# Performance work log

Measured on AMD Instinct MI355X. Metric: run time of the kernel, lower is better.

## Reference

```python
import jax, jax.numpy as jnp
import numpy as np

N_NODES = 100000
N_EDGES = 1000000
VOCAB = 105
OUT_DIM = 16
HIDDEN = 128


def setup_inputs() -> dict:
    key = jax.random.key(0)
    ks = jax.random.split(key, 9)
    x = jax.random.randint(ks[0], (N_NODES,), 0, VOCAB)
    pair_basis = jax.random.normal(ks[1], (N_EDGES, OUT_DIM), dtype=jnp.float32)
    i = jax.random.randint(ks[2], (N_EDGES,), 0, N_NODES)
    j = jax.random.randint(ks[3], (N_EDGES,), 0, N_NODES)
    # parameters
    emb_table = jax.random.normal(ks[4], (VOCAB, HIDDEN), dtype=jnp.float32)
    W_pair = jax.random.normal(ks[5], (OUT_DIM, HIDDEN), dtype=jnp.float32) / np.sqrt(OUT_DIM)
    b_pair = jnp.zeros((HIDDEN,), dtype=jnp.float32)
    W_emb = jax.random.normal(ks[6], (3 * HIDDEN, HIDDEN), dtype=jnp.float32) / np.sqrt(3 * HIDDEN)
    b_emb = jnp.zeros((HIDDEN,), dtype=jnp.float32)
    return {
        "x": x, "pair_basis": pair_basis, "i": i, "j": j,
        "emb_table": emb_table, "W_pair": W_pair, "b_pair": b_pair,
        "W_emb": W_emb, "b_emb": b_emb,
    }


def reference(x, pair_basis, i, j, emb_table, W_pair, b_pair, W_emb, b_emb):
    xe = emb_table[x]                                   # [N_nodes, H] embedding lookup
    pb = jax.nn.silu(pair_basis @ W_pair + b_pair)      # [E, H]
    inp = jnp.concatenate([xe[i], xe[j], pb], axis=-1)  # [E, 3H]
    emb = jax.nn.silu(inp @ W_emb + b_emb)              # [E, H]
    return emb
```

## Files before the change

### kernel.cpp

```cpp
#include <hip/hip_runtime.h>
#include <hip/hip_bf16.h>

#define N_EDGES 1000000
#define HID 128
#define VOC 105

#define WSU_T   0
#define WSU_U   (VOC * HID)
#define WSU_W3  (2 * VOC * HID)
#define WSU_WP  (WSU_W3 + 16384)
#define WSU_TU  (2 * VOC * HID)
#define WSB_VI  ((WSU_WP + 4096) * 2)
#define WSB_VJ  (WSB_VI + N_EDGES)

typedef float    f32x4 __attribute__((ext_vector_type(4)));
typedef _Float16 f16x8 __attribute__((ext_vector_type(8)));
typedef _Float16 f16x4 __attribute__((ext_vector_type(4)));

static __device__ __forceinline__ f16x8 as_f16x8(f32x4 v) {
    return __builtin_bit_cast(f16x8, v);
}
static __device__ __forceinline__ unsigned int pk2(float a, float b) {
    return __builtin_bit_cast(unsigned int, __builtin_amdgcn_cvt_pkrtz(a, b));
}

__global__ void prep_kernel(const int*   __restrict__ xv,
                            const int*   __restrict__ ii,
                            const int*   __restrict__ jj,
                            const float* __restrict__ emb_table,
                            const float* __restrict__ W_pair,
                            const float* __restrict__ b_pair,
                            const float* __restrict__ W_emb,
                            const float* __restrict__ b_emb,
                            char* __restrict__ wsb) {
    _Float16* ws = (_Float16*)wsb;
    int b = blockIdx.x, t = threadIdx.x;
    if (b < VOC) {
        int v = b, which = t >> 7, h = t & 127;
        const float* wr = W_emb + which * HID * HID;
        const float* ev = emb_table + v * HID;
        float acc = which ? 0.f : b_emb[h];
        for (int d = 0; d < HID; ++d) acc = fmaf(ev[d], wr[d * HID + h], acc);
        ws[(which ? WSU_U : WSU_T) + v * HID + h] = (_Float16)acc;
    } else if (b < VOC + 64) {
        int idx = (b - VOC) * 256 + t;
        int tt = idx & 7, lane = (idx >> 3) & 63, q = idx >> 9;
        int ks = q >> 3, nf = q & 7;
        int hl = 16 * (tt >> 2) + 4 * (lane >> 4) + (tt & 3);
        int k = 32 * ks + hl;
        int p = lane & 15;
        int n = (nf < 4) ? (4 * p + nf) : (64 + 4 * p + (nf - 4));
        ws[WSU_W3 + idx] = (_Float16)W_emb[(2 * HID + k) * HID + n];
    } else if (b < VOC + 64 + 16) {
        int idx = (b - VOC - 64) * 256 + t;
        int tt = idx & 7, lane = (idx >> 3) & 63, hf = idx >> 9;
        int k = 8 * (lane >> 4) + tt;
        int h = 16 * hf + (lane & 15);
        float v = (k < 16) ? W_pair[k * HID + h] : (k == 16 ? b_pair[h] : 0.f);
        ws[WSU_WP + idx] = (_Float16)v;
    } else {
        int e4 = ((b - VOC - 64 - 16) * 256 + t) * 4;
        if (e4 < N_EDGES) {
            int4 iv = *(const int4*)(ii + e4);
            int4 jv = *(const int4*)(jj + e4);
            unsigned int vi = (unsigned)xv[iv.x] | ((unsigned)xv[iv.y] << 8) |
                              ((unsigned)xv[iv.z] << 16) | ((unsigned)xv[iv.w] << 24);
            unsigned int vj = (unsigned)xv[jv.x] | ((unsigned)xv[jv.y] << 8) |
                              ((unsigned)xv[jv.z] << 16) | ((unsigned)xv[jv.w] << 24);
            *(unsigned int*)(wsb + WSB_VI + e4) = vi;
            *(unsigned int*)(wsb + WSB_VJ + e4) = vj;
        }
    }
}

__device__ __forceinline__ float silu_f(float x) {
    return x * __builtin_amdgcn_rcpf(1.f + __builtin_amdgcn_exp2f(-1.44269504088896341f * x));
}

__global__ __launch_bounds__(256, 2) void edge_kernel(
    const float* __restrict__ pair_basis,
    const char*  __restrict__ wsb,
    float* __restrict__ out)
{
    __shared__ __align__(16) _Float16 sTU[WSU_TU];
    const _Float16* ws = (const _Float16*)wsb;
    const int tid = threadIdx.x;
    {
        const uint4* src = (const uint4*)ws;
        uint4* dst = (uint4*)sTU;
        for (int c = tid; c < (WSU_TU * 2 / 16); c += 256) dst[c] = src[c];
    }
    const int lane = tid & 63;
    const int w    = tid >> 6;
    const int m    = lane & 15;
    const int g    = lane >> 4;

    f32x4 wpf[8];
    #pragma unroll
    for (int hf = 0; hf < 8; ++hf)
        wpf[hf] = *(const f32x4*)(ws + WSU_WP + (hf * 64 + lane) * 8);
    f32x4 w3r[32];
    #pragma unroll
    for (int q = 0; q < 32; ++q)
        w3r[q] = *(const f32x4*)(ws + WSU_W3 + (q * 64 + lane) * 8);
    #pragma unroll
    for (int hf = 0; hf < 8; ++hf) asm volatile("" : "+v"(wpf[hf]));
    #pragma unroll
    for (int q = 0; q < 32; ++q)  asm volatile("" : "+v"(w3r[q]));
    __syncthreads();

    const _Float16* sT  = sTU;
    const _Float16* sU  = sTU + WSU_U;
    const unsigned char* viB = (const unsigned char*)(wsb + WSB_VI);
    const unsigned char* vjB = (const unsigned char*)(wsb + WSB_VJ);

    const int ntiles = N_EDGES / 64;
    const int gstep  = (int)gridDim.x;

    int tile = blockIdx.x;
    if (tile >= ntiles) return;

    f32x4 p0 = {0,0,0,0}, p1 = {0,0,0,0};
    unsigned int viq, vjq;
    {
        int e0 = tile * 64 + w * 16;
        if (g < 2) {
            const f32x4* pr = (const f32x4*)(pair_basis + (size_t)(e0 + m) * 16 + g * 8);
            p0 = __builtin_nontemporal_load(pr);
            p1 = __builtin_nontemporal_load(pr + 1);
        }
        viq = *(const unsigned int*)(viB + e0 + 4 * g);
        vjq = *(const unsigned int*)(vjB + e0 + 4 * g);
    }

    while (true) {
        const int e0 = tile * 64 + w * 16;
        const int nt = tile + gstep;

        f32x4 q0 = {0,0,0,0}, q1 = {0,0,0,0};
        unsigned int nvi = 0, nvj = 0;
        if (nt < ntiles) {
            int ne0 = nt * 64 + w * 16;
            if (g < 2) {
                const f32x4* pr = (const f32x4*)(pair_basis + (size_t)(ne0 + m) * 16 + g * 8);
                q0 = __builtin_nontemporal_load(pr);
                q1 = __builtin_nontemporal_load(pr + 1);
            }
            nvi = *(const unsigned int*)(viB + ne0 + 4 * g);
            nvj = *(const unsigned int*)(vjB + ne0 + 4 * g);
        }

        f16x8 b2 = {0, 0, 0, 0, 0, 0, 0, 0};
        if (g < 2) {
            uint4 packed = {pk2(p0[0], p0[1]), pk2(p0[2], p0[3]),
                            pk2(p1[0], p1[1]), pk2(p1[2], p1[3])};
            b2 = __builtin_bit_cast(f16x8, packed);
        } else if (g == 2) {
            b2[0] = (_Float16)1.0f;
        }

        f16x8 a2[4];
        const f32x4 zero = {0.f, 0.f, 0.f, 0.f};
        #pragma unroll
        for (int ks = 0; ks < 4; ++ks) {
            f32x4 dA = __builtin_amdgcn_mfma_f32_16x16x32_f16(as_f16x8(wpf[2 * ks]),     b2, zero, 0, 0, 0);
            f32x4 dB = __builtin_amdgcn_mfma_f32_16x16x32_f16(as_f16x8(wpf[2 * ks + 1]), b2, zero, 0, 0, 0);
            uint4 packed;
            packed.x = pk2(silu_f(dA[0]), silu_f(dA[1]));
            packed.y = pk2(silu_f(dA[2]), silu_f(dA[3]));
            packed.z = pk2(silu_f(dB[0]), silu_f(dB[1]));
            packed.w = pk2(silu_f(dB[2]), silu_f(dB[3]));
            a2[ks] = __builtin_bit_cast(f16x8, packed);
        }

        f32x4 acc[8];
        #pragma unroll
        for (int r = 0; r < 4; ++r) {
            int vi = (viq >> (8 * r)) & 0xff;
            int vj = (vjq >> (8 * r)) & 0xff;
            f16x4 tlo = *(const f16x4*)(sT + vi * HID + 4 * m);
            f16x4 thi = *(const f16x4*)(sT + vi * HID + 64 + 4 * m);
            f16x4 ulo = *(const f16x4*)(sU + vj * HID + 4 * m);
            f16x4 uhi = *(const f16x4*)(sU + vj * HID + 64 + 4 * m);
            f16x4 slo = tlo + ulo;
            f16x4 shi = thi + uhi;
            #pragma unroll
            for (int nf = 0; nf < 4; ++nf) {
                acc[nf][r]     = (float)slo[nf];
                acc[4 + nf][r] = (float)shi[nf];
            }
        }

        #pragma unroll
        for (int ks = 0; ks < 4; ++ks) {
            #pragma unroll
            for (int nf = 0; nf < 8; ++nf)
                acc[nf] = __builtin_amdgcn_mfma_f32_16x16x32_f16(a2[ks], as_f16x8(w3r[ks * 8 + nf]), acc[nf], 0, 0, 0);
        }

        #pragma unroll
        for (int r = 0; r < 4; ++r) {
            float* op = out + (size_t)(e0 + 4 * g + r) * HID + 4 * m;
            f32x4 o0, o1;
            #pragma unroll
            for (int nf = 0; nf < 4; ++nf) {
                o0[nf] = silu_f(acc[nf][r]);
                o1[nf] = silu_f(acc[4 + nf][r]);
            }
            __builtin_nontemporal_store(o0, (f32x4*)op);
            __builtin_nontemporal_store(o1, (f32x4*)(op + 64));
        }

        if (nt >= ntiles) break;
        tile = nt; p0 = q0; p1 = q1; viq = nvi; vjq = nvj;
    }
}

extern "C" void kernel_launch(void* const* d_in, const int* in_sizes, int n_in,
                              void* d_out, int out_size, void* d_ws, size_t ws_size,
                              hipStream_t stream) {
    const int*   x          = (const int*)d_in[0];
    const float* pair_basis = (const float*)d_in[1];
    const int*   ii         = (const int*)d_in[2];
    const int*   jj         = (const int*)d_in[3];
    const float* emb_table  = (const float*)d_in[4];
    const float* W_pair     = (const float*)d_in[5];
    const float* b_pair     = (const float*)d_in[6];
    const float* W_emb      = (const float*)d_in[7];
    const float* b_emb      = (const float*)d_in[8];
    char* wsb = (char*)d_ws;
    float* out = (float*)d_out;

    const int ngather = (N_EDGES + 1023) / 1024;
    prep_kernel<<<VOC + 64 + 16 + ngather, 256, 0, stream>>>(
        x, ii, jj, emb_table, W_pair, b_pair, W_emb, b_emb, wsb);
    edge_kernel<<<512, 256, 0, stream>>>(pair_basis, wsb, out);
}
```

Baseline: 147.9 us.

## Move W_emb fragments from registers to LDS and use 1024-thread blocks

The 32 W3 weight fragments that were held in registers (128 VGPRs per thread) are now staged in shared memory together with the T/U tables and W_pair, and are read from LDS inside the MFMA loop. Blocks grow to 1024 threads (16 waves), with launch bounds of 4 blocks per unit, and the grid drops to 256 blocks, each wave striding over 16-edge tiles on its own. The aim is to cut register pressure so more waves fit and memory latency for the store-bound output is better hidden. In exchange, every tile now does extra LDS reads for the weights, and the larger LDS footprint per block may limit occupancy.

```diff
diff --git a/kernel.cpp b/kernel.cpp
--- a/kernel.cpp
+++ b/kernel.cpp
@@ -9,8 +9,8 @@
 #define WSU_U   (VOC * HID)
 #define WSU_W3  (2 * VOC * HID)
 #define WSU_WP  (WSU_W3 + 16384)
-#define WSU_TU  (2 * VOC * HID)
-#define WSB_VI  ((WSU_WP + 4096) * 2)
+#define WSU_ALL (WSU_WP + 4096)
+#define WSB_VI  (WSU_ALL * 2)
 #define WSB_VJ  (WSB_VI + N_EDGES)
 
 typedef float    f32x4 __attribute__((ext_vector_type(4)));
@@ -77,53 +77,48 @@
     return x * __builtin_amdgcn_rcpf(1.f + __builtin_amdgcn_exp2f(-1.44269504088896341f * x));
 }
 
-__global__ __launch_bounds__(256, 2) void edge_kernel(
+__global__ __launch_bounds__(1024, 4) void edge_kernel(
     const float* __restrict__ pair_basis,
     const char*  __restrict__ wsb,
     float* __restrict__ out)
 {
-    __shared__ __align__(16) _Float16 sTU[WSU_TU];
+    __shared__ __align__(16) _Float16 sAll[WSU_ALL];
     const _Float16* ws = (const _Float16*)wsb;
     const int tid = threadIdx.x;
     {
         const uint4* src = (const uint4*)ws;
-        uint4* dst = (uint4*)sTU;
-        for (int c = tid; c < (WSU_TU * 2 / 16); c += 256) dst[c] = src[c];
+        uint4* dst = (uint4*)sAll;
+        for (int c = tid; c < (WSU_ALL * 2 / 16); c += 1024) dst[c] = src[c];
     }
     const int lane = tid & 63;
     const int w    = tid >> 6;
     const int m    = lane & 15;
     const int g    = lane >> 4;
 
+    const _Float16* sT  = sAll;
+    const _Float16* sU  = sAll + WSU_U;
+    const _Float16* sW3 = sAll + WSU_W3;
+    const _Float16* sWP = sAll + WSU_WP;
+    const unsigned char* viB = (const unsigned char*)(wsb + WSB_VI);
+    const unsigned char* vjB = (const unsigned char*)(wsb + WSB_VJ);
+    __syncthreads();
+
     f32x4 wpf[8];
     #pragma unroll
     for (int hf = 0; hf < 8; ++hf)
-        wpf[hf] = *(const f32x4*)(ws + WSU_WP + (hf * 64 + lane) * 8);
-    f32x4 w3r[32];
-    #pragma unroll
-    for (int q = 0; q < 32; ++q)
-        w3r[q] = *(const f32x4*)(ws + WSU_W3 + (q * 64 + lane) * 8);
+        wpf[hf] = *(const f32x4*)(sWP + (hf * 64 + lane) * 8);
     #pragma unroll
     for (int hf = 0; hf < 8; ++hf) asm volatile("" : "+v"(wpf[hf]));
-    #pragma unroll
-    for (int q = 0; q < 32; ++q)  asm volatile("" : "+v"(w3r[q]));
-    __syncthreads();
-
-    const _Float16* sT  = sTU;
-    const _Float16* sU  = sTU + WSU_U;
-    const unsigned char* viB = (const unsigned char*)(wsb + WSB_VI);
-    const unsigned char* vjB = (const unsigned char*)(wsb + WSB_VJ);
-
-    const int ntiles = N_EDGES / 64;
-    const int gstep  = (int)gridDim.x;
-
-    int tile = blockIdx.x;
-    if (tile >= ntiles) return;
+
+    const int nwt   = N_EDGES / 16;
+    const int wstep = (int)gridDim.x * 16;
+    int wt = blockIdx.x * 16 + w;
+    if (wt >= nwt) return;
 
     f32x4 p0 = {0,0,0,0}, p1 = {0,0,0,0};
     unsigned int viq, vjq;
     {
-        int e0 = tile * 64 + w * 16;
+        int e0 = wt * 16;
         if (g < 2) {
             const f32x4* pr = (const f32x4*)(pair_basis + (size_t)(e0 + m) * 16 + g * 8);
             p0 = __builtin_nontemporal_load(pr);
@@ -134,13 +129,13 @@
     }
 
     while (true) {
-        const int e0 = tile * 64 + w * 16;
-        const int nt = tile + gstep;
+        const int e0 = wt * 16;
+        const int nt = wt + wstep;
 
         f32x4 q0 = {0,0,0,0}, q1 = {0,0,0,0};
         unsigned int nvi = 0, nvj = 0;
-        if (nt < ntiles) {
-            int ne0 = nt * 64 + w * 16;
+        if (nt < nwt) {
+            int ne0 = nt * 16;
             if (g < 2) {
                 const f32x4* pr = (const f32x4*)(pair_basis + (size_t)(ne0 + m) * 16 + g * 8);
                 q0 = __builtin_nontemporal_load(pr);
@@ -194,8 +189,10 @@
         #pragma unroll
         for (int ks = 0; ks < 4; ++ks) {
             #pragma unroll
-            for (int nf = 0; nf < 8; ++nf)
-                acc[nf] = __builtin_amdgcn_mfma_f32_16x16x32_f16(a2[ks], as_f16x8(w3r[ks * 8 + nf]), acc[nf], 0, 0, 0);
+            for (int nf = 0; nf < 8; ++nf) {
+                f16x8 bf = *(const f16x8*)(sW3 + ((ks * 8 + nf) * 64 + lane) * 8);
+                acc[nf] = __builtin_amdgcn_mfma_f32_16x16x32_f16(a2[ks], bf, acc[nf], 0, 0, 0);
+            }
         }
 
         #pragma unroll
@@ -211,8 +208,8 @@
             __builtin_nontemporal_store(o1, (f32x4*)(op + 64));
         }
 
-        if (nt >= ntiles) break;
-        tile = nt; p0 = q0; p1 = q1; viq = nvi; vjq = nvj;
+        if (nt >= nwt) break;
+        wt = nt; p0 = q0; p1 = q1; viq = nvi; vjq = nvj;
     }
 }
 
@@ -234,5 +231,5 @@
     const int ngather = (N_EDGES + 1023) / 1024;
     prep_kernel<<<VOC + 64 + 16 + ngather, 256, 0, stream>>>(
         x, ii, jj, emb_table, W_pair, b_pair, W_emb, b_emb, wsb);
-    edge_kernel<<<512, 256, 0, stream>>>(pair_basis, wsb, out);
-}
+    edge_kernel<<<256, 1024, 0, stream>>>(pair_basis, wsb, out);
+}
```

After: 373.5 us. +152.5%, slower.
